# Kernel tuning notes

Measured on AMD Instinct MI355X. Metric: run time of the kernel, lower is better.

## Reference

```python
import jax, jax.numpy as jnp
import numpy as np

TARGET_DIM, DRUG_DIM, INT_DIM, HID = 1024, 128, 128, 32
LN_EPS = 1e-5  # torch nn.LayerNorm default (module's eps arg is unused for LN)


def _layernorm(x, g, b):
    mu = jnp.mean(x, axis=-1, keepdims=True)
    var = jnp.var(x, axis=-1, keepdims=True)
    return (x - mu) * jax.lax.rsqrt(var + LN_EPS) * g + b


def setup_inputs() -> dict:
    key = jax.random.key(0)
    ks = jax.random.split(key, 10)
    B, NR, NA = 4, 512, 64
    s_t = 1.0 / np.sqrt(TARGET_DIM)
    s_d = 1.0 / np.sqrt(DRUG_DIM)
    s_o = 1.0 / np.sqrt(HID * HID)
    return {
        "target_embedding": jax.random.normal(ks[0], (B, NR, TARGET_DIM), jnp.float32),
        "drug_embedding": jax.random.normal(ks[1], (B, NA, DRUG_DIM), jnp.float32),
        "target_mask": jnp.ones((B, NR), jnp.float32),
        "drug_mask": jnp.ones((B, NA), jnp.float32),
        "ln_t_g": jnp.ones((TARGET_DIM,), jnp.float32),
        "ln_t_b": jnp.zeros((TARGET_DIM,), jnp.float32),
        "ln_d_g": jnp.ones((DRUG_DIM,), jnp.float32),
        "ln_d_b": jnp.zeros((DRUG_DIM,), jnp.float32),
        "W_t": jax.random.uniform(ks[2], (HID, TARGET_DIM), jnp.float32, -s_t, s_t),
        "b_t": jax.random.uniform(ks[3], (HID,), jnp.float32, -s_t, s_t),
        "W_d": jax.random.uniform(ks[4], (HID, DRUG_DIM), jnp.float32, -s_d, s_d),
        "b_d": jax.random.uniform(ks[5], (HID,), jnp.float32, -s_d, s_d),
        "W_out": jax.random.uniform(ks[6], (INT_DIM, HID * HID), jnp.float32, -s_o, s_o),
        "b_out": jax.random.uniform(ks[7], (INT_DIM,), jnp.float32, -s_o, s_o),
    }


def reference(target_embedding, drug_embedding, target_mask, drug_mask,
              ln_t_g, ln_t_b, ln_d_g, ln_d_b, W_t, b_t, W_d, b_d, W_out, b_out):
    t = _layernorm(target_embedding, ln_t_g, ln_t_b)
    d = _layernorm(drug_embedding, ln_d_g, ln_d_b)
    # projections + mask: [B,NR,H], [B,NA,H]
    tf = (t @ W_t.T + b_t) * target_mask[..., None]
    df = (d @ W_d.T + b_d) * drug_mask[..., None]
    # fused outer-product + linear_out: W_out row index i over flat (c*H+e)
    W3 = W_out.reshape(INT_DIM, HID, HID)  # [i, c, e]
    outer = jnp.einsum('bnc,bme,ice->bnmi', tf, df, W3) + b_out
    mask = target_mask[:, :, None] * drug_mask[:, None, :]  # [B,NR,NA]
    outer = outer * mask[..., None]
    return outer, mask
```

## Files before the change

### kernel.cpp

```cpp
#include <hip/hip_runtime.h>

typedef __attribute__((ext_vector_type(8))) short short8;
typedef __attribute__((ext_vector_type(4))) float f32x4;

#define LNP_YSTRIDE 1032
#define GSTR 1048

__device__ __forceinline__ unsigned short f2bf(float f) {
  union { float f; unsigned u; } v; v.f = f;
  unsigned r = v.u + 0x7FFFu + ((v.u >> 16) & 1u);
  return (unsigned short)(r >> 16);
}
__device__ __forceinline__ unsigned pack2(float a, float b) {
  return (unsigned)f2bf(a) | ((unsigned)f2bf(b) << 16);
}
__device__ __forceinline__ short8 packW(float4 a, float4 b) {
  union { short8 s; unsigned u[4]; } r;
  r.u[0] = pack2(a.x, a.y); r.u[1] = pack2(a.z, a.w);
  r.u[2] = pack2(b.x, b.y); r.u[3] = pack2(b.z, b.w);
  return r.s;
}

__device__ __forceinline__ void lnproj8_t(
    const float* __restrict__ X, const float* __restrict__ g, const float* __restrict__ bia,
    const float* __restrict__ W, const float* __restrict__ pb, const float* __restrict__ msk,
    unsigned short* __restrict__ outb, int row0, unsigned short* Yl, float* pd, int tid)
{
  const int w = tid >> 6, lid = tid & 63, l = tid & 15, q = (tid >> 4) & 3;
  const f32x4 zero = {0.f, 0.f, 0.f, 0.f};

  #pragma unroll
  for (int rr = 0; rr < 2; ++rr) {
    const int row = w * 2 + rr;
    const float* xr = X + (size_t)(row0 + row) * 1024;
    float4 v[4];
    float s = 0.f, s2 = 0.f;
    #pragma unroll
    for (int k = 0; k < 4; ++k) {
      v[k] = *(const float4*)(xr + 4 * lid + 256 * k);
      s  += (v[k].x + v[k].y) + (v[k].z + v[k].w);
      s2 += (v[k].x * v[k].x + v[k].y * v[k].y) + (v[k].z * v[k].z + v[k].w * v[k].w);
    }
    #pragma unroll
    for (int off = 32; off >= 1; off >>= 1) { s += __shfl_xor(s, off, 64); s2 += __shfl_xor(s2, off, 64); }
    const float mu = s * (1.f / 1024.f);
    const float rs = rsqrtf(s2 * (1.f / 1024.f) - mu * mu + 1e-5f);
    #pragma unroll
    for (int k = 0; k < 4; ++k) {
      float4 gg = *(const float4*)(g + 4 * lid + 256 * k);
      float4 bb = *(const float4*)(bia + 4 * lid + 256 * k);
      unsigned* yd = (unsigned*)(Yl + row * LNP_YSTRIDE + 4 * lid + 256 * k);
      yd[0] = pack2((v[k].x - mu) * rs * gg.x + bb.x, (v[k].y - mu) * rs * gg.y + bb.y);
      yd[1] = pack2((v[k].z - mu) * rs * gg.z + bb.z, (v[k].w - mu) * rs * gg.w + bb.w);
    }
  }
  __syncthreads();

  f32x4 acc0 = zero, acc1 = zero;
  #pragma unroll
  for (int ss = 0; ss < 8; ++ss) {
    const int s = w * 8 + ss;
    short8 af = *(const short8*)(Yl + l * LNP_YSTRIDE + s * 32 + q * 8);
    const float* wp0 = W + (size_t)l * 1024 + s * 32 + q * 8;
    const float* wp1 = W + (size_t)(16 + l) * 1024 + s * 32 + q * 8;
    acc0 = __builtin_amdgcn_mfma_f32_16x16x32_bf16(af, packW(*(const float4*)wp0, *(const float4*)(wp0 + 4)), acc0, 0, 0, 0);
    acc1 = __builtin_amdgcn_mfma_f32_16x16x32_bf16(af, packW(*(const float4*)wp1, *(const float4*)(wp1 + 4)), acc1, 0, 0, 0);
  }
  if (w > 0 && q < 2) {
    #pragma unroll
    for (int r = 0; r < 4; ++r) {
      const int rl = q * 4 + r;
      pd[(w - 1) * 256 + rl * 16 + l]       = acc0[r];
      pd[(w - 1) * 256 + 128 + rl * 16 + l] = acc1[r];
    }
  }
  __syncthreads();
  if (w == 0 && q < 2) {
    #pragma unroll
    for (int ht = 0; ht < 2; ++ht) {
      const int h = ht * 16 + l;
      const float pbv = pb[h];
      #pragma unroll
      for (int r = 0; r < 4; ++r) {
        const int rl = q * 4 + r, rg = row0 + rl;
        float val = (ht ? acc1[r] : acc0[r]) + pbv;
        #pragma unroll
        for (int k = 0; k < 3; ++k) val += pd[k * 256 + ht * 128 + rl * 16 + l];
        outb[(size_t)rg * 32 + h] = f2bf(val * msk[rg]);
      }
    }
  }
}

template<int ROWLEN>
__device__ __forceinline__ void lnproj(
    const float* __restrict__ X, const float* __restrict__ g, const float* __restrict__ bia,
    const float* __restrict__ W, const float* __restrict__ pb, const float* __restrict__ msk,
    unsigned short* __restrict__ outb, int row0, unsigned short* Yl, float* pd, int tid)
{
  const int w = tid >> 6, lid = tid & 63, l = tid & 15, q = (tid >> 4) & 3;

  #pragma unroll
  for (int rr = 0; rr < 4; ++rr) {
    const int row = w * 4 + rr;
    const float* xr = X + (size_t)(row0 + row) * ROWLEN;
    float2 v = *(const float2*)(xr + 2 * lid);
    float s = v.x + v.y, s2 = v.x * v.x + v.y * v.y;
    #pragma unroll
    for (int off = 32; off >= 1; off >>= 1) { s += __shfl_xor(s, off, 64); s2 += __shfl_xor(s2, off, 64); }
    const float mu = s * (1.f / ROWLEN);
    const float rs = rsqrtf(s2 * (1.f / ROWLEN) - mu * mu + 1e-5f);
    float2 gg = *(const float2*)(g + 2 * lid);
    float2 bb = *(const float2*)(bia + 2 * lid);
    *(unsigned*)(Yl + row * LNP_YSTRIDE + 2 * lid) =
        pack2((v.x - mu) * rs * gg.x + bb.x, (v.y - mu) * rs * gg.y + bb.y);
  }
  __syncthreads();

  const int KST = ROWLEN / 32;
  const int ht = w & 1, kh = w >> 1;
  const int h = ht * 16 + l;
  f32x4 acc = {0.f, 0.f, 0.f, 0.f};
  #pragma unroll
  for (int s = kh * (KST / 2); s < kh * (KST / 2) + KST / 2; ++s) {
    short8 af = *(const short8*)(Yl + l * LNP_YSTRIDE + s * 32 + q * 8);
    const float* wp = W + (size_t)h * ROWLEN + s * 32 + q * 8;
    short8 bf = packW(*(const float4*)wp, *(const float4*)(wp + 4));
    acc = __builtin_amdgcn_mfma_f32_16x16x32_bf16(af, bf, acc, 0, 0, 0);
  }
  if (w >= 2) {
    #pragma unroll
    for (int r = 0; r < 4; ++r) pd[ht * 256 + (q * 4 + r) * 16 + l] = acc[r];
  }
  __syncthreads();
  if (w < 2) {
    const float pbv = pb[h];
    #pragma unroll
    for (int r = 0; r < 4; ++r) {
      const int rg = row0 + q * 4 + r;
      float val = acc[r] + pd[ht * 256 + (q * 4 + r) * 16 + l] + pbv;
      val *= msk[rg];
      outb[(size_t)rg * 32 + h] = f2bf(val);
    }
  }
}

__global__ __launch_bounds__(256) void k_pre(
    const float* __restrict__ tgt, const float* __restrict__ drg,
    const float* __restrict__ tmask, const float* __restrict__ dmask,
    const float* __restrict__ ln_t_g, const float* __restrict__ ln_t_b,
    const float* __restrict__ ln_d_g, const float* __restrict__ ln_d_b,
    const float* __restrict__ W_t, const float* __restrict__ b_t,
    const float* __restrict__ W_d, const float* __restrict__ b_d,
    const float* __restrict__ W_out,
    unsigned short* __restrict__ w3pp, unsigned short* __restrict__ tfb,
    unsigned short* __restrict__ dfb, float* __restrict__ mask_out)
{
  __shared__ unsigned short Yl[16 * LNP_YSTRIDE];
  __shared__ float pd[3 * 256];
  const int blk = blockIdx.x, tid = threadIdx.x;
  if (blk < 256) {
    lnproj8_t(tgt, ln_t_g, ln_t_b, W_t, b_t, tmask, tfb, blk * 8, Yl, pd, tid);
  } else if (blk < 272) {
    lnproj<128>(drg, ln_d_g, ln_d_b, W_d, b_d, dmask, dfb, (blk - 256) * 16, Yl, pd, tid);
  } else if (blk < 280) {
    const int tg = (blk - 272) * 256 + tid;
    #pragma unroll
    for (int rep = 0; rep < 2; ++rep) {
      const int f = tg + rep * 2048;
      const int i = f >> 5, e = f & 31;
      unsigned short us[32];
      #pragma unroll
      for (int c = 0; c < 32; ++c) us[c] = f2bf(W_out[i * 1024 + c * 32 + e]);
      unsigned* dst = (unsigned*)(w3pp + (size_t)f * 32);
      #pragma unroll
      for (int j = 0; j < 16; ++j) dst[j] = (unsigned)us[2 * j] | ((unsigned)us[2 * j + 1] << 16);
    }
  } else {
    const int base = ((blk - 280) * 256 + tid) * 4;
    const int b = base >> 15;
    const float tm = tmask[base >> 6];
    float4 d = *(const float4*)(dmask + b * 64 + (base & 63));
    float4 o; o.x = tm * d.x; o.y = tm * d.y; o.z = tm * d.z; o.w = tm * d.w;
    *(float4*)(mask_out + base) = o;
  }
}

__global__ __launch_bounds__(256) void k_main(
    const unsigned short* __restrict__ w3pp, const unsigned short* __restrict__ tfb,
    const unsigned short* __restrict__ dfb, const float* __restrict__ b_out,
    const float* __restrict__ tmask, const float* __restrict__ dmask,
    float* __restrict__ out)
{
  __shared__ unsigned short Gl[16 * GSTR];
  const int id = blockIdx.x;
  const int b = id >> 7, n16 = (id >> 2) & 31, iq = id & 3;
  const int n0 = n16 * 16, i0 = iq * 32;
  const int tid = threadIdx.x, w = tid >> 6, l = tid & 15, q = (tid >> 4) & 3;

  short8 atf = *(const short8*)(tfb + (size_t)(b * 512 + n0 + l) * 32 + q * 8);
  short8 bdf[4];
  #pragma unroll
  for (int mt = 0; mt < 4; ++mt)
    bdf[mt] = *(const short8*)(dfb + (size_t)(b * 64 + mt * 16 + l) * 32 + q * 8);

  const f32x4 zero = {0.f, 0.f, 0.f, 0.f};

  for (int t = w * 16; t < w * 16 + 16; ++t) {
    const int f = i0 * 32 + t * 16 + l;
    short8 bw = *(const short8*)(w3pp + (size_t)f * 32 + q * 8);
    f32x4 d = __builtin_amdgcn_mfma_f32_16x16x32_bf16(atf, bw, zero, 0, 0, 0);
    const int floc = t * 16 + l, ip = floc >> 5, e = floc & 31;
    #pragma unroll
    for (int r = 0; r < 4; ++r)
      Gl[(q * 4 + r) * GSTR + ip * 32 + e] = f2bf(d[r]);
  }
  __syncthreads();

  const float4 bo0 = *(const float4*)(b_out + i0 + q * 4);
  const float4 bo1 = *(const float4*)(b_out + i0 + 16 + q * 4);
  float dm[4];
  #pragma unroll
  for (int mt = 0; mt < 4; ++mt) dm[mt] = dmask[b * 64 + mt * 16 + l];

  for (int j = 0; j < 8; ++j) {
    const int p = w * 8 + j, n = p >> 1, it = p & 1;
    short8 ag = *(const short8*)(Gl + n * GSTR + (it * 16 + l) * 32 + q * 8);
    const float tmv = tmask[b * 512 + n0 + n];
    const float4 bo = it ? bo1 : bo0;
    const size_t obase = ((size_t)(b * 512 + n0 + n) * 64) * 128 + (size_t)(i0 + it * 16 + q * 4);
    #pragma unroll
    for (int mt = 0; mt < 4; ++mt) {
      f32x4 d = __builtin_amdgcn_mfma_f32_16x16x32_bf16(ag, bdf[mt], zero, 0, 0, 0);
      const float s = tmv * dm[mt];
      float4 o;
      o.x = (d[0] + bo.x) * s; o.y = (d[1] + bo.y) * s;
      o.z = (d[2] + bo.z) * s; o.w = (d[3] + bo.w) * s;
      *(float4*)(out + obase + (size_t)(mt * 16 + l) * 128) = o;
    }
  }
}

extern "C" void kernel_launch(void* const* d_in, const int* in_sizes, int n_in,
                              void* d_out, int out_size, void* d_ws, size_t ws_size,
                              hipStream_t stream)
{
  const float* tgt    = (const float*)d_in[0];
  const float* drg    = (const float*)d_in[1];
  const float* tmask  = (const float*)d_in[2];
  const float* dmask  = (const float*)d_in[3];
  const float* ln_t_g = (const float*)d_in[4];
  const float* ln_t_b = (const float*)d_in[5];
  const float* ln_d_g = (const float*)d_in[6];
  const float* ln_d_b = (const float*)d_in[7];
  const float* W_t    = (const float*)d_in[8];
  const float* b_t    = (const float*)d_in[9];
  const float* W_d    = (const float*)d_in[10];
  const float* b_d    = (const float*)d_in[11];
  const float* W_out  = (const float*)d_in[12];
  const float* b_out  = (const float*)d_in[13];

  float* out = (float*)d_out;
  float* mask_out = out + (size_t)4 * 512 * 64 * 128;

  char* ws = (char*)d_ws;
  unsigned short* w3pp = (unsigned short*)(ws);
  unsigned short* tfb  = (unsigned short*)(ws + 262144);
  unsigned short* dfb  = (unsigned short*)(ws + 262144 + 131072);

  k_pre<<<dim3(408), dim3(256), 0, stream>>>(
      tgt, drg, tmask, dmask, ln_t_g, ln_t_b, ln_d_g, ln_d_b,
      W_t, b_t, W_d, b_d, W_out, w3pp, tfb, dfb, mask_out);
  k_main<<<dim3(512), dim3(256), 0, stream>>>(
      w3pp, tfb, dfb, b_out, tmask, dmask, out);
}
```

Before: 114.9 us.

## Contract drug features with W_out first, then multiply by target features

Changes the contraction order. A new middle kernel computes H[b,m,i,c] = sum_e W_out[i,c,e]*df[b,m,e] in bf16, and the main kernel then does one MFMA per tile against tf, which removes the LDS staging and the barrier. This avoids the per-block recomputation of the W_out·tf intermediate and the W_out repacking in k_pre, and adds nontemporal output stores. The cost is an extra kernel launch, a 2MB intermediate round trip through global memory, and an additional bf16 rounding of H.

```diff
diff --git a/kernel.cpp b/kernel.cpp
--- a/kernel.cpp
+++ b/kernel.cpp
@@ -4,7 +4,6 @@
 typedef __attribute__((ext_vector_type(4))) float f32x4;
 
 #define LNP_YSTRIDE 1032
-#define GSTR 1048
 
 __device__ __forceinline__ unsigned short f2bf(float f) {
   union { float f; unsigned u; } v; v.f = f;
@@ -152,9 +151,8 @@
     const float* __restrict__ ln_d_g, const float* __restrict__ ln_d_b,
     const float* __restrict__ W_t, const float* __restrict__ b_t,
     const float* __restrict__ W_d, const float* __restrict__ b_d,
-    const float* __restrict__ W_out,
-    unsigned short* __restrict__ w3pp, unsigned short* __restrict__ tfb,
-    unsigned short* __restrict__ dfb, float* __restrict__ mask_out)
+    unsigned short* __restrict__ tfb, unsigned short* __restrict__ dfb,
+    float* __restrict__ mask_out)
 {
   __shared__ unsigned short Yl[16 * LNP_YSTRIDE];
   __shared__ float pd[3 * 256];
@@ -163,21 +161,8 @@
     lnproj8_t(tgt, ln_t_g, ln_t_b, W_t, b_t, tmask, tfb, blk * 8, Yl, pd, tid);
   } else if (blk < 272) {
     lnproj<128>(drg, ln_d_g, ln_d_b, W_d, b_d, dmask, dfb, (blk - 256) * 16, Yl, pd, tid);
-  } else if (blk < 280) {
-    const int tg = (blk - 272) * 256 + tid;
-    #pragma unroll
-    for (int rep = 0; rep < 2; ++rep) {
-      const int f = tg + rep * 2048;
-      const int i = f >> 5, e = f & 31;
-      unsigned short us[32];
-      #pragma unroll
-      for (int c = 0; c < 32; ++c) us[c] = f2bf(W_out[i * 1024 + c * 32 + e]);
-      unsigned* dst = (unsigned*)(w3pp + (size_t)f * 32);
-      #pragma unroll
-      for (int j = 0; j < 16; ++j) dst[j] = (unsigned)us[2 * j] | ((unsigned)us[2 * j + 1] << 16);
-    }
   } else {
-    const int base = ((blk - 280) * 256 + tid) * 4;
+    const int base = ((blk - 272) * 256 + tid) * 4;
     const int b = base >> 15;
     const float tm = tmask[base >> 6];
     float4 d = *(const float4*)(dmask + b * 64 + (base & 63));
@@ -186,58 +171,68 @@
   }
 }
 
+__global__ __launch_bounds__(256) void k_mid(
+    const float* __restrict__ W_out, const unsigned short* __restrict__ dfb,
+    unsigned short* __restrict__ Hb)
+{
+  const int id = blockIdx.x;
+  const int b = id >> 6, icg = id & 63;
+  const int tid = threadIdx.x, w = tid >> 6, l = tid & 15, q = (tid >> 4) & 3;
+  const f32x4 zero = {0.f, 0.f, 0.f, 0.f};
+  const int m = w * 16 + l;
+  short8 bf = *(const short8*)(dfb + (size_t)(b * 64 + m) * 32 + q * 8);
+  #pragma unroll
+  for (int u = 0; u < 4; ++u) {
+    const int ic0 = icg * 64 + u * 16;
+    const float* ap = W_out + (size_t)(ic0 + l) * 32 + q * 8;
+    short8 af = packW(*(const float4*)ap, *(const float4*)(ap + 4));
+    f32x4 d = __builtin_amdgcn_mfma_f32_16x16x32_bf16(af, bf, zero, 0, 0, 0);
+    uint2 hv; hv.x = pack2(d[0], d[1]); hv.y = pack2(d[2], d[3]);
+    *(uint2*)(Hb + (size_t)(b * 64 + m) * 4096 + ic0 + q * 4) = hv;
+  }
+}
+
 __global__ __launch_bounds__(256) void k_main(
-    const unsigned short* __restrict__ w3pp, const unsigned short* __restrict__ tfb,
-    const unsigned short* __restrict__ dfb, const float* __restrict__ b_out,
-    const float* __restrict__ tmask, const float* __restrict__ dmask,
-    float* __restrict__ out)
-{
-  __shared__ unsigned short Gl[16 * GSTR];
+    const unsigned short* __restrict__ Hb, const unsigned short* __restrict__ tfb,
+    const float* __restrict__ b_out, const float* __restrict__ tmask,
+    const float* __restrict__ dmask, float* __restrict__ out)
+{
   const int id = blockIdx.x;
-  const int b = id >> 7, n16 = (id >> 2) & 31, iq = id & 3;
-  const int n0 = n16 * 16, i0 = iq * 32;
+  const int b = id >> 9, m = (id >> 3) & 63, ng = id & 7;
   const int tid = threadIdx.x, w = tid >> 6, l = tid & 15, q = (tid >> 4) & 3;
-
-  short8 atf = *(const short8*)(tfb + (size_t)(b * 512 + n0 + l) * 32 + q * 8);
-  short8 bdf[4];
-  #pragma unroll
-  for (int mt = 0; mt < 4; ++mt)
-    bdf[mt] = *(const short8*)(dfb + (size_t)(b * 64 + mt * 16 + l) * 32 + q * 8);
-
+  const int n0 = ng * 64;
   const f32x4 zero = {0.f, 0.f, 0.f, 0.f};
 
-  for (int t = w * 16; t < w * 16 + 16; ++t) {
-    const int f = i0 * 32 + t * 16 + l;
-    short8 bw = *(const short8*)(w3pp + (size_t)f * 32 + q * 8);
-    f32x4 d = __builtin_amdgcn_mfma_f32_16x16x32_bf16(atf, bw, zero, 0, 0, 0);
-    const int floc = t * 16 + l, ip = floc >> 5, e = floc & 31;
-    #pragma unroll
-    for (int r = 0; r < 4; ++r)
-      Gl[(q * 4 + r) * GSTR + ip * 32 + e] = f2bf(d[r]);
-  }
-  __syncthreads();
-
-  const float4 bo0 = *(const float4*)(b_out + i0 + q * 4);
-  const float4 bo1 = *(const float4*)(b_out + i0 + 16 + q * 4);
-  float dm[4];
-  #pragma unroll
-  for (int mt = 0; mt < 4; ++mt) dm[mt] = dmask[b * 64 + mt * 16 + l];
-
-  for (int j = 0; j < 8; ++j) {
-    const int p = w * 8 + j, n = p >> 1, it = p & 1;
-    short8 ag = *(const short8*)(Gl + n * GSTR + (it * 16 + l) * 32 + q * 8);
-    const float tmv = tmask[b * 512 + n0 + n];
-    const float4 bo = it ? bo1 : bo0;
-    const size_t obase = ((size_t)(b * 512 + n0 + n) * 64) * 128 + (size_t)(i0 + it * 16 + q * 4);
-    #pragma unroll
-    for (int mt = 0; mt < 4; ++mt) {
-      f32x4 d = __builtin_amdgcn_mfma_f32_16x16x32_bf16(ag, bdf[mt], zero, 0, 0, 0);
-      const float s = tmv * dm[mt];
-      float4 o;
-      o.x = (d[0] + bo.x) * s; o.y = (d[1] + bo.y) * s;
-      o.z = (d[2] + bo.z) * s; o.w = (d[3] + bo.w) * s;
-      *(float4*)(out + obase + (size_t)(mt * 16 + l) * 128) = o;
-    }
+  const unsigned short* hrow = Hb + (size_t)(b * 64 + m) * 4096;
+  short8 a0 = *(const short8*)(hrow + (w * 32 + l) * 32 + q * 8);
+  short8 a1 = *(const short8*)(hrow + (w * 32 + 16 + l) * 32 + q * 8);
+
+  short8 bfr[4];
+  #pragma unroll
+  for (int t2 = 0; t2 < 4; ++t2)
+    bfr[t2] = *(const short8*)(tfb + (size_t)(b * 512 + n0 + t2 * 16 + l) * 32 + q * 8);
+
+  const float4 bo0 = *(const float4*)(b_out + w * 32 + q * 4);
+  const float4 bo1 = *(const float4*)(b_out + w * 32 + 16 + q * 4);
+  const float dmv = dmask[b * 64 + m];
+  float tmv[4];
+  #pragma unroll
+  for (int t2 = 0; t2 < 4; ++t2)
+    tmv[t2] = tmask[b * 512 + n0 + t2 * 16 + l] * dmv;
+
+  #pragma unroll
+  for (int t2 = 0; t2 < 4; ++t2) {
+    const size_t rbase = ((size_t)(b * 512 + n0 + t2 * 16 + l) * 64 + m) * 128;
+    const float s = tmv[t2];
+    f32x4 d0 = __builtin_amdgcn_mfma_f32_16x16x32_bf16(a0, bfr[t2], zero, 0, 0, 0);
+    f32x4 d1 = __builtin_amdgcn_mfma_f32_16x16x32_bf16(a1, bfr[t2], zero, 0, 0, 0);
+    f32x4 o0, o1;
+    o0[0] = (d0[0] + bo0.x) * s; o0[1] = (d0[1] + bo0.y) * s;
+    o0[2] = (d0[2] + bo0.z) * s; o0[3] = (d0[3] + bo0.w) * s;
+    o1[0] = (d1[0] + bo1.x) * s; o1[1] = (d1[1] + bo1.y) * s;
+    o1[2] = (d1[2] + bo1.z) * s; o1[3] = (d1[3] + bo1.w) * s;
+    __builtin_nontemporal_store(o0, (f32x4*)(out + rbase + w * 32 + q * 4));
+    __builtin_nontemporal_store(o1, (f32x4*)(out + rbase + w * 32 + 16 + q * 4));
   }
 }
 
@@ -264,13 +259,13 @@
   float* mask_out = out + (size_t)4 * 512 * 64 * 128;
 
   char* ws = (char*)d_ws;
-  unsigned short* w3pp = (unsigned short*)(ws);
-  unsigned short* tfb  = (unsigned short*)(ws + 262144);
-  unsigned short* dfb  = (unsigned short*)(ws + 262144 + 131072);
-
-  k_pre<<<dim3(408), dim3(256), 0, stream>>>(
+  unsigned short* Hb  = (unsigned short*)(ws);
+  unsigned short* tfb = (unsigned short*)(ws + 2097152);
+  unsigned short* dfb = (unsigned short*)(ws + 2097152 + 131072);
+
+  k_pre<<<dim3(400), dim3(256), 0, stream>>>(
       tgt, drg, tmask, dmask, ln_t_g, ln_t_b, ln_d_g, ln_d_b,
-      W_t, b_t, W_d, b_d, W_out, w3pp, tfb, dfb, mask_out);
-  k_main<<<dim3(512), dim3(256), 0, stream>>>(
-      w3pp, tfb, dfb, b_out, tmask, dmask, out);
-}
+      W_t, b_t, W_d, b_d, tfb, dfb, mask_out);
+  k_mid<<<dim3(256), dim3(256), 0, stream>>>(W_out, dfb, Hb);
+  k_main<<<dim3(2048), dim3(256), 0, stream>>>(Hb, tfb, b_out, tmask, dmask, out);
+}
```

Result: slower. 122.9 us (+7.0%).
